# Kernel tuning notes

Hardware: AMD Instinct MI355X
Metric: run time of the kernel (lower is better)

The kernel has to match this reference:

```python
import jax, jax.numpy as jnp
import numpy as np

ALPHA = 0.5
BETA = 0.5
N_NODES = 100000
N_EDGES = 1600000
D = 64  # out_channels


def setup_inputs() -> dict:
    key = jax.random.key(0)
    ks = jax.random.split(key, 8)
    z_in = jax.random.normal(ks[0], (N_NODES, D + 1), dtype=jnp.float32)
    z_out = jax.random.normal(ks[1], (N_NODES, D + 1), dtype=jnp.float32)
    z_self = jax.random.normal(ks[2], (N_NODES, D), dtype=jnp.float32)
    edge_index = jax.random.randint(ks[3], (2, N_EDGES), 0, N_NODES, dtype=jnp.int64)
    s = 1.0 / np.sqrt(D)  # torch Linear default init scale
    W_in = jax.random.uniform(ks[4], (D, D), jnp.float32, -s, s)
    b_in = jax.random.uniform(ks[5], (D,), jnp.float32, -s, s)
    W_out = jax.random.uniform(ks[6], (D, D), jnp.float32, -s, s)
    b_out = jax.random.uniform(ks[7], (D,), jnp.float32, -s, s)
    return {"z_in": z_in, "z_out": z_out, "z_self": z_self,
            "W_in": W_in, "b_in": b_in, "W_out": W_out, "b_out": b_out,
            "edge_index": edge_index}


def _norm_degree(deg, n_unique):
    # degree / (num_unique_nodes - 1), then L2-normalize over dim 0 (F.normalize)
    d = deg / (n_unique - 1.0)
    nrm = jnp.maximum(jnp.linalg.norm(d), 1e-12)
    return d / nrm


def reference(z_in, z_out, z_self, W_in, b_in, W_out, b_out, edge_index):
    src = edge_index[0]
    dst = edge_index[1]
    n = z_self.shape[0]
    ones = jnp.ones(src.shape, jnp.float32)
    deg_out = jax.ops.segment_sum(ones, src, num_segments=n)  # out-degree per node
    deg_in = jax.ops.segment_sum(ones, dst, num_segments=n)   # in-degree per node
    present = jnp.zeros((n,), bool).at[edge_index.reshape(-1)].set(True)
    n_unique = present.sum().astype(jnp.float32)  # len(set(edge_index.flatten()))
    real_degreeout = _norm_degree(deg_out, n_unique)[src]  # [E]
    real_degreein = _norm_degree(deg_in, n_unique)[dst]    # [E]
    # small aligned linears on gathered node features
    align_out_dst = z_self[dst] @ W_out.T + b_out  # [E, D]
    align_in_src = z_self[src] @ W_in.T + b_in     # [E, D]
    value = ((real_degreeout + z_out[src, -1]) * BETA
             + jnp.sum(z_out[src, :-1] * align_out_dst, axis=1) * ALPHA
             + (real_degreein + z_in[dst, -1]) * BETA
             + jnp.sum(align_in_src * z_in[dst, :-1], axis=1) * ALPHA)
    return jax.nn.sigmoid(value)
```

## Files before the change

kernel.cpp:

```cpp
#include <hip/hip_runtime.h>
#include <hip/hip_fp16.h>
#include <math.h>

#define ALPHA_C 0.5f
#define BETA_C  0.5f
#define NPART   256
#define NQUART  4

typedef _Float16 half8 __attribute__((ext_vector_type(8)));
typedef _Float16 half2v __attribute__((ext_vector_type(2)));
typedef float f32x4 __attribute__((ext_vector_type(4)));

__device__ __forceinline__ int swz(int row, int byteoff) {
    return byteoff ^ ((row & 7) << 4);
}

__global__ __launch_bounds__(256) void k_prep(
        const float* __restrict__ W_in, const float* __restrict__ W_out,
        _Float16* __restrict__ w16i, _Float16* __restrict__ w16o) {
    for (int i = threadIdx.x; i < 4096; i += 256) {
        int k = i >> 6, n = i & 63;
        w16o[n * 64 + k] = (_Float16)W_out[k * 64 + n];
        w16i[n * 64 + k] = (_Float16)W_in [k * 64 + n];
    }
}

__global__ __launch_bounds__(256) void k_hist(
        const int* __restrict__ eidx, unsigned int* __restrict__ scr,
        int N, int E, int Q, int Wd, int chunk) {
    const int s = blockIdx.x;
    const int role = blockIdx.y;
    const int dir = role & 1;
    const int q = role >> 1;
    extern __shared__ unsigned int lds[];
    for (int w = threadIdx.x; w < Wd; w += blockDim.x) lds[w] = 0;
    __syncthreads();
    const int base = q * Q;
    const int hi = min(N - base, Q);
    const int* __restrict__ arr = eidx + (size_t)dir * E;
    const int start = s * chunk;
    const int end = min(E, start + chunk);
    const int4* __restrict__ a4 = (const int4*)arr;
    const int v1 = end >> 2;
    for (int v = (start >> 2) + threadIdx.x; v < v1; v += blockDim.x) {
        int4 x = a4[v];
        int l;
        l = x.x - base; if ((unsigned)l < (unsigned)hi) atomicAdd(&lds[l >> 1], 1u << ((l & 1) * 16));
        l = x.y - base; if ((unsigned)l < (unsigned)hi) atomicAdd(&lds[l >> 1], 1u << ((l & 1) * 16));
        l = x.z - base; if ((unsigned)l < (unsigned)hi) atomicAdd(&lds[l >> 1], 1u << ((l & 1) * 16));
        l = x.w - base; if ((unsigned)l < (unsigned)hi) atomicAdd(&lds[l >> 1], 1u << ((l & 1) * 16));
    }
    for (int i = (v1 << 2) + threadIdx.x; i < end; i += blockDim.x) {
        int l = arr[i] - base;
        if ((unsigned)l < (unsigned)hi) atomicAdd(&lds[l >> 1], 1u << ((l & 1) * 16));
    }
    __syncthreads();
    unsigned int* __restrict__ dst = scr + ((size_t)role * gridDim.x + s) * Wd;
    for (int w = threadIdx.x; w < Wd; w += blockDim.x) dst[w] = lds[w];
}

__global__ __launch_bounds__(256) void k_fold(
        const unsigned int* __restrict__ scr,
        float* __restrict__ deg_out, float* __restrict__ deg_in,
        float* __restrict__ partials, int N, int Q, int Wd, int S) {
    float so = 0.f, si = 0.f;
    for (int n = blockIdx.x * blockDim.x + threadIdx.x; n < N;
         n += gridDim.x * blockDim.x) {
        const int q = n / Q, l = n - q * Q;
        const int w = l >> 1, sh = (l & 1) * 16;
        const unsigned int* __restrict__ p0 = scr + ((size_t)(q * 2 + 0) * S) * Wd + w;
        const unsigned int* __restrict__ p1 = scr + ((size_t)(q * 2 + 1) * S) * Wd + w;
        unsigned int a = 0, b = 0;
        for (int s = 0; s < S; ++s) {
            a += (p0[(size_t)s * Wd] >> sh) & 0xFFFFu;
            b += (p1[(size_t)s * Wd] >> sh) & 0xFFFFu;
        }
        float fa = (float)a, fb = (float)b;
        deg_out[n] = fa;
        deg_in[n] = fb;
        so = fmaf(fa, fa, so);
        si = fmaf(fb, fb, si);
    }
#pragma unroll
    for (int off = 32; off; off >>= 1) {
        so += __shfl_xor(so, off);
        si += __shfl_xor(si, off);
    }
    __shared__ float sm[2][4];
    int lane = threadIdx.x & 63, w = threadIdx.x >> 6;
    if (lane == 0) { sm[0][w] = so; sm[1][w] = si; }
    __syncthreads();
    if (threadIdx.x == 0) {
        partials[blockIdx.x]         = sm[0][0] + sm[0][1] + sm[0][2] + sm[0][3];
        partials[NPART + blockIdx.x] = sm[1][0] + sm[1][1] + sm[1][2] + sm[1][3];
    }
}

__global__ __launch_bounds__(256) void k_finish(
        const float* __restrict__ partials, float* __restrict__ inv_nrm) {
    int t = threadIdx.x;
    float so = partials[t], si = partials[NPART + t];
#pragma unroll
    for (int off = 32; off; off >>= 1) {
        so += __shfl_xor(so, off);
        si += __shfl_xor(si, off);
    }
    __shared__ float sm[2][4];
    int lane = t & 63, w = t >> 6;
    if (lane == 0) { sm[0][w] = so; sm[1][w] = si; }
    __syncthreads();
    if (t == 0) {
        float a = sm[0][0] + sm[0][1] + sm[0][2] + sm[0][3];
        float b = sm[1][0] + sm[1][1] + sm[1][2] + sm[1][3];
        inv_nrm[0] = (a > 0.f) ? rsqrtf(a) : 0.f;
        inv_nrm[1] = (b > 0.f) ? rsqrtf(b) : 0.f;
    }
}

__global__ __launch_bounds__(256) void k_nodes(
        const float* __restrict__ z_in, const float* __restrict__ z_out,
        const float* __restrict__ z_self,
        const _Float16* __restrict__ w16i, const _Float16* __restrict__ w16o,
        const float* __restrict__ b_in, const float* __restrict__ b_out,
        const float* __restrict__ deg_out, const float* __restrict__ deg_in,
        const float* __restrict__ inv_nrm,
        _Float16* __restrict__ P_src, _Float16* __restrict__ P_dst,
        float* __restrict__ s_src, float* __restrict__ s_dst, int N) {
    __shared__ _Float16 smem[16384];
    char* lzo = (char*)smem;
    char* lzi = (char*)smem + 8192;
    char* lps = (char*)smem;
    char* lpd = (char*)smem + 16384;

    const int tid = threadIdx.x;
    const int lane = tid & 63;
    const int wid = tid >> 6;
    const int r = lane & 15, g = lane >> 4;
    const int base = blockIdx.x * 64;
    const int wrow = wid * 16;

#pragma unroll
    for (int it = 0; it < 8; ++it) {
        int flat = it * 256 + tid;
        int row = flat >> 5;
        int c2 = (flat & 31) * 2;
        int grow = min(base + row, N - 1);
        const float* zr = z_out + (size_t)grow * 65;
        half2v ho = { (_Float16)zr[c2], (_Float16)zr[c2 + 1] };
        *(half2v*)(lzo + row * 128 + swz(row, c2 * 2)) = ho;
        const float* zr2 = z_in + (size_t)grow * 65;
        half2v hi = { (_Float16)zr2[c2], (_Float16)zr2[c2 + 1] };
        *(half2v*)(lzi + row * 128 + swz(row, c2 * 2)) = hi;
    }
    half8 bO[2], bI[2];
#pragma unroll
    for (int s = 0; s < 2; ++s)
#pragma unroll
        for (int j = 0; j < 8; ++j) {
            int k = 32 * s + 8 * g + j;
            bO[s][j] = (r == 0) ? (_Float16)b_out[k] : (_Float16)0.f;
            bI[s][j] = (r == 0) ? (_Float16)b_in [k] : (_Float16)0.f;
        }
    __syncthreads();

    half8 AO[2], AI[2];
#pragma unroll
    for (int s = 0; s < 2; ++s) {
        int arow = wrow + r;
        int off = arow * 128 + swz(arow, s * 64 + g * 16);
        AO[s] = *(half8*)(lzo + off);
        AI[s] = *(half8*)(lzi + off);
    }
    f32x4 aO[4], aI[4], abO = (f32x4)0.f, abI = (f32x4)0.f;
#pragma unroll
    for (int t = 0; t < 4; ++t) { aO[t] = (f32x4)0.f; aI[t] = (f32x4)0.f; }
#pragma unroll
    for (int s = 0; s < 2; ++s) {
#pragma unroll
        for (int t = 0; t < 4; ++t) {
            int woff = (16 * t + r) * 64 + 32 * s + 8 * g;
            half8 BO = *(const half8*)(w16o + woff);
            aO[t] = __builtin_amdgcn_mfma_f32_16x16x32_f16(AO[s], BO, aO[t], 0, 0, 0);
            half8 BI = *(const half8*)(w16i + woff);
            aI[t] = __builtin_amdgcn_mfma_f32_16x16x32_f16(AI[s], BI, aI[t], 0, 0, 0);
        }
        abO = __builtin_amdgcn_mfma_f32_16x16x32_f16(AO[s], bO[s], abO, 0, 0, 0);
        abI = __builtin_amdgcn_mfma_f32_16x16x32_f16(AI[s], bI[s], abI, 0, 0, 0);
    }
    __syncthreads();

#pragma unroll
    for (int t = 0; t < 4; ++t)
#pragma unroll
        for (int rr = 0; rr < 4; ++rr) {
            int lrow = wrow + 4 * g + rr;
            int col2 = (16 * t + r) * 2;
            *(_Float16*)(lps + lrow * 256 + swz(lrow, col2)) = (_Float16)aO[t][rr];
            *(_Float16*)(lpd + lrow * 256 + swz(lrow, 128 + col2)) = (_Float16)aI[t][rr];
        }
#pragma unroll
    for (int it = 0; it < 8; ++it) {
        int flat = it * 256 + tid;
        int row = flat >> 5;
        int c2 = (flat & 31) * 2;
        int grow = min(base + row, N - 1);
        float2 v = *(const float2*)(z_self + (size_t)grow * 64 + c2);
        half2v h = { (_Float16)v.x, (_Float16)v.y };
        *(half2v*)(lps + row * 256 + swz(row, 128 + c2 * 2)) = h;
        *(half2v*)(lpd + row * 256 + swz(row, c2 * 2)) = h;
    }
    if (r == 0) {
        const float i0 = inv_nrm[0], i1 = inv_nrm[1];
#pragma unroll
        for (int rr = 0; rr < 4; ++rr) {
            int m = base + wrow + 4 * g + rr;
            if (m < N) {
                s_src[m] = BETA_C * fmaf(deg_out[m], i0, z_out[(size_t)m * 65 + 64])
                         + ALPHA_C * abO[rr];
                s_dst[m] = BETA_C * fmaf(deg_in[m],  i1, z_in [(size_t)m * 65 + 64])
                         + ALPHA_C * abI[rr];
            }
        }
    }
    __syncthreads();

#pragma unroll
    for (int it = 0; it < 4; ++it) {
        int lrow = it * 16 + (tid >> 4);
        int seg = tid & 15;
        int m = base + lrow;
        if (m < N) {
            half8 v = *(half8*)(lps + lrow * 256 + swz(lrow, seg * 16));
            *(half8*)(P_src + (size_t)m * 128 + seg * 8) = v;
            half8 v2 = *(half8*)(lpd + lrow * 256 + swz(lrow, seg * 16));
            *(half8*)(P_dst + (size_t)m * 128 + seg * 8) = v2;
        }
    }
}

__global__ __launch_bounds__(256) void k_edges(
        const int* __restrict__ eidx,
        const _Float16* __restrict__ P_src, const _Float16* __restrict__ P_dst,
        const float* __restrict__ s_src, const float* __restrict__ s_dst,
        float* __restrict__ out, int E) {
    const int sub = threadIdx.x & 15;
    const int grp = blockIdx.x * (blockDim.x >> 4) + (threadIdx.x >> 4);
    const int e0 = grp << 1;
    if (e0 >= E) return;
    const bool has1 = (e0 + 1) < E;
    int2 ss = *(const int2*)(eidx + e0);
    int2 dd = *(const int2*)(eidx + E + e0);
    const int s1 = has1 ? ss.y : ss.x, d1 = has1 ? dd.y : dd.x;
    const uint4 a0 = *(const uint4*)(P_src + (size_t)ss.x * 128 + sub * 8);
    const uint4 b0 = *(const uint4*)(P_dst + (size_t)dd.x * 128 + sub * 8);
    const uint4 a1 = *(const uint4*)(P_src + (size_t)s1 * 128 + sub * 8);
    const uint4 b1 = *(const uint4*)(P_dst + (size_t)d1 * 128 + sub * 8);
    float ssum = 0.f;
    if (sub < 2) {
        int s = sub ? s1 : ss.x;
        int d = sub ? d1 : dd.x;
        ssum = s_src[s] + s_dst[d];
    }
    float acc0 = 0.f, acc1 = 0.f;
    acc0 = __builtin_amdgcn_fdot2(__builtin_bit_cast(half2v, a0.x), __builtin_bit_cast(half2v, b0.x), acc0, false);
    acc0 = __builtin_amdgcn_fdot2(__builtin_bit_cast(half2v, a0.y), __builtin_bit_cast(half2v, b0.y), acc0, false);
    acc0 = __builtin_amdgcn_fdot2(__builtin_bit_cast(half2v, a0.z), __builtin_bit_cast(half2v, b0.z), acc0, false);
    acc0 = __builtin_amdgcn_fdot2(__builtin_bit_cast(half2v, a0.w), __builtin_bit_cast(half2v, b0.w), acc0, false);
    acc1 = __builtin_amdgcn_fdot2(__builtin_bit_cast(half2v, a1.x), __builtin_bit_cast(half2v, b1.x), acc1, false);
    acc1 = __builtin_amdgcn_fdot2(__builtin_bit_cast(half2v, a1.y), __builtin_bit_cast(half2v, b1.y), acc1, false);
    acc1 = __builtin_amdgcn_fdot2(__builtin_bit_cast(half2v, a1.z), __builtin_bit_cast(half2v, b1.z), acc1, false);
    acc1 = __builtin_amdgcn_fdot2(__builtin_bit_cast(half2v, a1.w), __builtin_bit_cast(half2v, b1.w), acc1, false);
#pragma unroll
    for (int off = 8; off; off >>= 1) {
        acc0 += __shfl_xor(acc0, off);
        acc1 += __shfl_xor(acc1, off);
    }
    if (sub < 2 && (sub == 0 || has1)) {
        float acc = sub ? acc1 : acc0;
        float v = fmaf(ALPHA_C, acc, ssum);
        out[e0 + sub] = 1.0f / (1.0f + __expf(-v));
    }
}

extern "C" void kernel_launch(void* const* d_in, const int* in_sizes, int n_in,
                              void* d_out, int out_size, void* d_ws, size_t ws_size,
                              hipStream_t stream) {
    const float* z_in   = (const float*)d_in[0];
    const float* z_out  = (const float*)d_in[1];
    const float* z_self = (const float*)d_in[2];
    const float* W_in   = (const float*)d_in[3];
    const float* b_in   = (const float*)d_in[4];
    const float* W_out  = (const float*)d_in[5];
    const float* b_out  = (const float*)d_in[6];
    const int*   eidx   = (const int*)d_in[7];

    const int N = in_sizes[2] / 64;
    const int E = in_sizes[7] / 2;

    const int Q = (N + NQUART - 1) / NQUART;
    const int Wd = (Q + 1) / 2;
    int S = (E + 49999) / 50000;
    if (S < 1) S = 1;
    int chunk = ((E + S - 1) / S + 3) & ~3;

    float* ws       = (float*)d_ws;
    float* deg_out  = ws;
    float* deg_in   = ws + (size_t)N;
    float* s_src    = ws + 2 * (size_t)N;
    float* s_dst    = ws + 3 * (size_t)N;
    _Float16* P_src = (_Float16*)(ws + 4 * (size_t)N);
    _Float16* P_dst = P_src + (size_t)N * 128;
    float* partials = (float*)(P_dst + (size_t)N * 128);
    float* inv_nrm  = partials + 2 * NPART;
    _Float16* w16o  = (_Float16*)(partials + 2 * NPART + 16);
    _Float16* w16i  = w16o + 4096;
    unsigned int* scr = (unsigned int*)P_src;

    k_prep<<<1, 256, 0, stream>>>(W_in, W_out, w16i, w16o);
    dim3 hgrid(S, 2 * NQUART);
    k_hist<<<hgrid, 256, (size_t)Wd * 4, stream>>>(eidx, scr, N, E, Q, Wd, chunk);
    k_fold<<<NPART, 256, 0, stream>>>(scr, deg_out, deg_in, partials, N, Q, Wd, S);
    k_finish<<<1, 256, 0, stream>>>(partials, inv_nrm);
    k_nodes<<<(N + 63) / 64, 256, 0, stream>>>(z_in, z_out, z_self, w16i, w16o,
                                               b_in, b_out, deg_out, deg_in,
                                               inv_nrm, P_src, P_dst,
                                               s_src, s_dst, N);
    {
        int groups = (E + 1) / 2;
        int blocks = (groups + 15) / 16;
        k_edges<<<blocks, 256, 0, stream>>>(eidx, P_src, P_dst,
                                            s_src, s_dst, (float*)d_out, E);
    }
}
```

Before: 212.9 us.

## Bucket edges by destination range for locality and fold weight prep into node kernel

Adds a counting pass and a scatter pass that reorder edges into eight buckets by destination-node range, packing src and the local dst offset into one word. A new edge kernel then processes each bucket so that P_dst gathers hit a smaller working set that may stay in cache. Separately, the one-block weight transpose/convert kernel is removed and each node block converts W into LDS itself. The cost is extra passes over the edge list, writes of packed indices plus permutation, and scattered output writes through eidq.

```diff
diff --git a/kernel.cpp b/kernel.cpp
--- a/kernel.cpp
+++ b/kernel.cpp
@@ -6,6 +6,8 @@
 #define BETA_C  0.5f
 #define NPART   256
 #define NQUART  4
+#define NBKT    8
+#define SCH     6250
 
 typedef _Float16 half8 __attribute__((ext_vector_type(8)));
 typedef _Float16 half2v __attribute__((ext_vector_type(2)));
@@ -13,16 +15,6 @@
 
 __device__ __forceinline__ int swz(int row, int byteoff) {
     return byteoff ^ ((row & 7) << 4);
-}
-
-__global__ __launch_bounds__(256) void k_prep(
-        const float* __restrict__ W_in, const float* __restrict__ W_out,
-        _Float16* __restrict__ w16i, _Float16* __restrict__ w16o) {
-    for (int i = threadIdx.x; i < 4096; i += 256) {
-        int k = i >> 6, n = i & 63;
-        w16o[n * 64 + k] = (_Float16)W_out[k * 64 + n];
-        w16i[n * 64 + k] = (_Float16)W_in [k * 64 + n];
-    }
 }
 
 __global__ __launch_bounds__(256) void k_hist(
@@ -57,6 +49,30 @@
     __syncthreads();
     unsigned int* __restrict__ dst = scr + ((size_t)role * gridDim.x + s) * Wd;
     for (int w = threadIdx.x; w < Wd; w += blockDim.x) dst[w] = lds[w];
+}
+
+__global__ __launch_bounds__(256) void k_bcnt(
+        const int* __restrict__ eidx, unsigned* __restrict__ wgcnt,
+        int E, int BQ) {
+    __shared__ unsigned cnt[NBKT];
+    if (threadIdx.x < NBKT) cnt[threadIdx.x] = 0;
+    __syncthreads();
+    const int c0 = blockIdx.x * SCH;
+    const int lim = min(E - c0, SCH);
+    const int lane = threadIdx.x & 63;
+    for (int it = 0; it * 256 < lim; ++it) {
+        int i = it * 256 + threadIdx.x;
+        unsigned bkt = NBKT;
+        if (i < lim) bkt = (unsigned)eidx[E + c0 + i] / (unsigned)BQ;
+#pragma unroll
+        for (unsigned b = 0; b < NBKT; ++b) {
+            unsigned long long m = __ballot(bkt == b);
+            if (m && lane == (__ffsll((long long)m) - 1))
+                atomicAdd(&cnt[b], (unsigned)__popcll(m));
+        }
+    }
+    __syncthreads();
+    if (threadIdx.x < NBKT) wgcnt[blockIdx.x * NBKT + threadIdx.x] = cnt[threadIdx.x];
 }
 
 __global__ __launch_bounds__(256) void k_fold(
@@ -97,8 +113,19 @@
 }
 
 __global__ __launch_bounds__(256) void k_finish(
-        const float* __restrict__ partials, float* __restrict__ inv_nrm) {
+        const float* __restrict__ partials, float* __restrict__ inv_nrm,
+        const unsigned* __restrict__ wgcnt, unsigned* __restrict__ wgbase,
+        unsigned* __restrict__ bmeta, int NWG) {
     int t = threadIdx.x;
+    __shared__ unsigned sb[NBKT];
+    if (t < NBKT && NWG > 0) {
+        unsigned run = 0;
+        for (int w = 0; w < NWG; ++w) {
+            wgbase[w * NBKT + t] = run;
+            run += wgcnt[w * NBKT + t];
+        }
+        sb[t] = run;
+    }
     float so = partials[t], si = partials[NPART + t];
 #pragma unroll
     for (int off = 32; off; off >>= 1) {
@@ -114,14 +141,66 @@
         float b = sm[1][0] + sm[1][1] + sm[1][2] + sm[1][3];
         inv_nrm[0] = (a > 0.f) ? rsqrtf(a) : 0.f;
         inv_nrm[1] = (b > 0.f) ? rsqrtf(b) : 0.f;
+        if (NWG > 0) {
+            unsigned acc = 0;
+#pragma unroll
+            for (int bb = 0; bb < NBKT; ++bb) {
+                bmeta[bb] = acc;
+                bmeta[NBKT + bb] = sb[bb];
+                acc += sb[bb];
+            }
+        }
+    }
+}
+
+__global__ __launch_bounds__(256) void k_scatter(
+        const int* __restrict__ eidx, const unsigned* __restrict__ wgbase,
+        const unsigned* __restrict__ bmeta, unsigned* __restrict__ packed_sd,
+        int* __restrict__ eidq, int E, int BQ) {
+    __shared__ unsigned lsd[SCH];
+    __shared__ unsigned char lb[SCH];
+    __shared__ unsigned lcur[NBKT];
+    const int w = blockIdx.x;
+    const int c0 = w * SCH;
+    const int lim = min(E - c0, SCH);
+    const int tid = threadIdx.x, lane = tid & 63;
+    if (tid < NBKT) lcur[tid] = bmeta[tid] + wgbase[w * NBKT + tid];
+    for (int it = 0; it * 256 < lim; ++it) {
+        int i = it * 256 + tid;
+        if (i < lim) {
+            unsigned s = (unsigned)eidx[c0 + i];
+            unsigned d = (unsigned)eidx[E + c0 + i];
+            unsigned b = d / (unsigned)BQ;
+            lsd[i] = s | ((d - b * (unsigned)BQ) << 17);
+            lb[i] = (unsigned char)b;
+        }
+    }
+    __syncthreads();
+    for (int it = 0; it * 256 < lim; ++it) {
+        int i = it * 256 + tid;
+        unsigned bkt = (i < lim) ? (unsigned)lb[i] : (unsigned)NBKT;
+#pragma unroll
+        for (unsigned b = 0; b < NBKT; ++b) {
+            unsigned long long m = __ballot(bkt == b);
+            if (!m) continue;
+            int leader = __ffsll((long long)m) - 1;
+            unsigned pbase = 0;
+            if (lane == leader) pbase = atomicAdd(&lcur[b], (unsigned)__popcll(m));
+            pbase = (unsigned)__shfl((int)pbase, leader);
+            if (bkt == b) {
+                unsigned pos = pbase + (unsigned)__popcll(m & ((1ULL << lane) - 1));
+                packed_sd[pos] = lsd[i];
+                eidq[pos] = c0 + i;
+            }
+        }
     }
 }
 
 __global__ __launch_bounds__(256) void k_nodes(
         const float* __restrict__ z_in, const float* __restrict__ z_out,
         const float* __restrict__ z_self,
-        const _Float16* __restrict__ w16i, const _Float16* __restrict__ w16o,
-        const float* __restrict__ b_in, const float* __restrict__ b_out,
+        const float* __restrict__ W_in, const float* __restrict__ b_in,
+        const float* __restrict__ W_out, const float* __restrict__ b_out,
         const float* __restrict__ deg_out, const float* __restrict__ deg_in,
         const float* __restrict__ inv_nrm,
         _Float16* __restrict__ P_src, _Float16* __restrict__ P_dst,
@@ -129,6 +208,8 @@
     __shared__ _Float16 smem[16384];
     char* lzo = (char*)smem;
     char* lzi = (char*)smem + 8192;
+    char* lwo = (char*)smem + 16384;
+    char* lwi = (char*)smem + 24576;
     char* lps = (char*)smem;
     char* lpd = (char*)smem + 16384;
 
@@ -152,6 +233,13 @@
         half2v hi = { (_Float16)zr2[c2], (_Float16)zr2[c2 + 1] };
         *(half2v*)(lzi + row * 128 + swz(row, c2 * 2)) = hi;
     }
+#pragma unroll
+    for (int it = 0; it < 16; ++it) {
+        int flat = it * 256 + tid;
+        int k = flat >> 6, n = flat & 63;
+        *(_Float16*)(lwo + n * 128 + swz(n, k * 2)) = (_Float16)W_out[k * 64 + n];
+        *(_Float16*)(lwi + n * 128 + swz(n, k * 2)) = (_Float16)W_in [k * 64 + n];
+    }
     half8 bO[2], bI[2];
 #pragma unroll
     for (int s = 0; s < 2; ++s)
@@ -178,10 +266,11 @@
     for (int s = 0; s < 2; ++s) {
 #pragma unroll
         for (int t = 0; t < 4; ++t) {
-            int woff = (16 * t + r) * 64 + 32 * s + 8 * g;
-            half8 BO = *(const half8*)(w16o + woff);
+            int n = 16 * t + r;
+            int off = n * 128 + swz(n, s * 64 + g * 16);
+            half8 BO = *(half8*)(lwo + off);
             aO[t] = __builtin_amdgcn_mfma_f32_16x16x32_f16(AO[s], BO, aO[t], 0, 0, 0);
-            half8 BI = *(const half8*)(w16i + woff);
+            half8 BI = *(half8*)(lwi + off);
             aI[t] = __builtin_amdgcn_mfma_f32_16x16x32_f16(AI[s], BI, aI[t], 0, 0, 0);
         }
         abO = __builtin_amdgcn_mfma_f32_16x16x32_f16(AO[s], bO[s], abO, 0, 0, 0);
@@ -234,6 +323,61 @@
             *(half8*)(P_src + (size_t)m * 128 + seg * 8) = v;
             half8 v2 = *(half8*)(lpd + lrow * 256 + swz(lrow, seg * 16));
             *(half8*)(P_dst + (size_t)m * 128 + seg * 8) = v2;
+        }
+    }
+}
+
+__global__ __launch_bounds__(256) void k_edges2(
+        const unsigned* __restrict__ packed_sd, const int* __restrict__ eidq,
+        const unsigned* __restrict__ bmeta,
+        const _Float16* __restrict__ P_src, const _Float16* __restrict__ P_dst,
+        const float* __restrict__ s_src, const float* __restrict__ s_dst,
+        float* __restrict__ out, int BQ) {
+    const int b = blockIdx.x & (NBKT - 1);
+    const unsigned base = bmeta[b], cnt = bmeta[NBKT + b];
+    const unsigned dbase = (unsigned)b * (unsigned)BQ;
+    const unsigned jstr = gridDim.x >> 3;
+    const int sub = threadIdx.x & 15;
+    const int grp = threadIdx.x >> 4;
+    for (unsigned j = blockIdx.x >> 3; j * 32 < cnt; j += jstr) {
+        unsigned i0 = j * 32 + (unsigned)grp * 2;
+        bool v0 = i0 < cnt, v1 = (i0 + 1) < cnt;
+        unsigned ce0 = base + (v0 ? i0 : 0u);
+        unsigned ce1 = base + (v1 ? i0 + 1 : (v0 ? i0 : 0u));
+        unsigned p0 = packed_sd[ce0], p1 = packed_sd[ce1];
+        int s0 = p0 & 0x1FFFF, d0 = (int)(dbase + (p0 >> 17));
+        int s1 = p1 & 0x1FFFF, d1 = (int)(dbase + (p1 >> 17));
+        const uint4 a0 = *(const uint4*)(P_src + (size_t)s0 * 128 + sub * 8);
+        const uint4 b0 = *(const uint4*)(P_dst + (size_t)d0 * 128 + sub * 8);
+        const uint4 a1 = *(const uint4*)(P_src + (size_t)s1 * 128 + sub * 8);
+        const uint4 b1 = *(const uint4*)(P_dst + (size_t)d1 * 128 + sub * 8);
+        float ssum = 0.f;
+        if (sub < 2) {
+            int s = sub ? s1 : s0;
+            int d = sub ? d1 : d0;
+            ssum = s_src[s] + s_dst[d];
+        }
+        float acc0 = 0.f, acc1 = 0.f;
+        acc0 = __builtin_amdgcn_fdot2(__builtin_bit_cast(half2v, a0.x), __builtin_bit_cast(half2v, b0.x), acc0, false);
+        acc0 = __builtin_amdgcn_fdot2(__builtin_bit_cast(half2v, a0.y), __builtin_bit_cast(half2v, b0.y), acc0, false);
+        acc0 = __builtin_amdgcn_fdot2(__builtin_bit_cast(half2v, a0.z), __builtin_bit_cast(half2v, b0.z), acc0, false);
+        acc0 = __builtin_amdgcn_fdot2(__builtin_bit_cast(half2v, a0.w), __builtin_bit_cast(half2v, b0.w), acc0, false);
+        acc1 = __builtin_amdgcn_fdot2(__builtin_bit_cast(half2v, a1.x), __builtin_bit_cast(half2v, b1.x), acc1, false);
+        acc1 = __builtin_amdgcn_fdot2(__builtin_bit_cast(half2v, a1.y), __builtin_bit_cast(half2v, b1.y), acc1, false);
+        acc1 = __builtin_amdgcn_fdot2(__builtin_bit_cast(half2v, a1.z), __builtin_bit_cast(half2v, b1.z), acc1, false);
+        acc1 = __builtin_amdgcn_fdot2(__builtin_bit_cast(half2v, a1.w), __builtin_bit_cast(half2v, b1.w), acc1, false);
+#pragma unroll
+        for (int off = 8; off; off >>= 1) {
+            acc0 += __shfl_xor(acc0, off);
+            acc1 += __shfl_xor(acc1, off);
+        }
+        if (sub == 0 && v0) {
+            float v = fmaf(ALPHA_C, acc0, ssum);
+            out[eidq[ce0]] = 1.0f / (1.0f + __expf(-v));
+        }
+        if (sub == 1 && v1) {
+            float v = fmaf(ALPHA_C, acc1, ssum);
+            out[eidq[ce1]] = 1.0f / (1.0f + __expf(-v));
         }
     }
 }
@@ -303,6 +447,9 @@
     if (S < 1) S = 1;
     int chunk = ((E + S - 1) / S + 3) & ~3;
 
+    const int BQ = (N + NBKT - 1) / NBKT;
+    const int NWG = (E + SCH - 1) / SCH;
+
     float* ws       = (float*)d_ws;
     float* deg_out  = ws;
     float* deg_in   = ws + (size_t)N;
@@ -312,20 +459,35 @@
     _Float16* P_dst = P_src + (size_t)N * 128;
     float* partials = (float*)(P_dst + (size_t)N * 128);
     float* inv_nrm  = partials + 2 * NPART;
-    _Float16* w16o  = (_Float16*)(partials + 2 * NPART + 16);
-    _Float16* w16i  = w16o + 4096;
+    unsigned* wgcnt = (unsigned*)(inv_nrm + 2);
+    unsigned* wgbase = wgcnt + (size_t)NWG * NBKT;
+    unsigned* bmeta  = wgbase + (size_t)NWG * NBKT;
+    unsigned* packed_sd = bmeta + 16;
+    int*      eidq      = (int*)(packed_sd + (size_t)E);
+    size_t need_bytes = (size_t)((char*)(eidq + (size_t)E) - (char*)d_ws);
+    const bool bucketed = (ws_size >= need_bytes) && (N <= (1 << 17));
     unsigned int* scr = (unsigned int*)P_src;
 
-    k_prep<<<1, 256, 0, stream>>>(W_in, W_out, w16i, w16o);
     dim3 hgrid(S, 2 * NQUART);
     k_hist<<<hgrid, 256, (size_t)Wd * 4, stream>>>(eidx, scr, N, E, Q, Wd, chunk);
+    if (bucketed)
+        k_bcnt<<<NWG, 256, 0, stream>>>(eidx, wgcnt, E, BQ);
     k_fold<<<NPART, 256, 0, stream>>>(scr, deg_out, deg_in, partials, N, Q, Wd, S);
-    k_finish<<<1, 256, 0, stream>>>(partials, inv_nrm);
-    k_nodes<<<(N + 63) / 64, 256, 0, stream>>>(z_in, z_out, z_self, w16i, w16o,
-                                               b_in, b_out, deg_out, deg_in,
+    k_finish<<<1, 256, 0, stream>>>(partials, inv_nrm, wgcnt, wgbase, bmeta,
+                                    bucketed ? NWG : 0);
+    if (bucketed)
+        k_scatter<<<NWG, 256, 0, stream>>>(eidx, wgbase, bmeta,
+                                           packed_sd, eidq, E, BQ);
+    k_nodes<<<(N + 63) / 64, 256, 0, stream>>>(z_in, z_out, z_self, W_in, b_in,
+                                               W_out, b_out, deg_out, deg_in,
                                                inv_nrm, P_src, P_dst,
                                                s_src, s_dst, N);
-    {
+    if (bucketed) {
+        int blocks = ((E + 31) / 32 + 7) & ~7;
+        k_edges2<<<blocks, 256, 0, stream>>>(packed_sd, eidq, bmeta,
+                                             P_src, P_dst, s_src, s_dst,
+                                             (float*)d_out, BQ);
+    } else {
         int groups = (E + 1) / 2;
         int blocks = (groups + 15) / 16;
         k_edges<<<blocks, 256, 0, stream>>>(eidx, P_src, P_dst,
```

Result: slower. 276.9 us (+30.1%).

## Fold weight prep into finish kernel, stage weights in LDS, 4 edges per group

Applied to the files above, without the earlier changes.

Removes the separate single-block weight-conversion launch by folding it into k_finish. k_nodes now stages the fp16 weight matrices in swizzled LDS instead of reading them from global memory per MFMA operand. k_edges processes four edges per 16-lane group instead of two, issuing more independent gathers per thread to raise memory-level parallelism, at the cost of more registers and scalar index loads. The LDS staging uses the upper half of the shared buffer, which later overlaps the output staging region after a sync.

```diff
diff --git a/kernel.cpp b/kernel.cpp
--- a/kernel.cpp
+++ b/kernel.cpp
@@ -13,16 +13,6 @@
 
 __device__ __forceinline__ int swz(int row, int byteoff) {
     return byteoff ^ ((row & 7) << 4);
-}
-
-__global__ __launch_bounds__(256) void k_prep(
-        const float* __restrict__ W_in, const float* __restrict__ W_out,
-        _Float16* __restrict__ w16i, _Float16* __restrict__ w16o) {
-    for (int i = threadIdx.x; i < 4096; i += 256) {
-        int k = i >> 6, n = i & 63;
-        w16o[n * 64 + k] = (_Float16)W_out[k * 64 + n];
-        w16i[n * 64 + k] = (_Float16)W_in [k * 64 + n];
-    }
 }
 
 __global__ __launch_bounds__(256) void k_hist(
@@ -97,8 +87,15 @@
 }
 
 __global__ __launch_bounds__(256) void k_finish(
-        const float* __restrict__ partials, float* __restrict__ inv_nrm) {
+        const float* __restrict__ partials, float* __restrict__ inv_nrm,
+        const float* __restrict__ W_in, const float* __restrict__ W_out,
+        _Float16* __restrict__ w16i, _Float16* __restrict__ w16o) {
     int t = threadIdx.x;
+    for (int i = t; i < 4096; i += 256) {
+        int k = i >> 6, n = i & 63;
+        w16o[n * 64 + k] = (_Float16)W_out[k * 64 + n];
+        w16i[n * 64 + k] = (_Float16)W_in [k * 64 + n];
+    }
     float so = partials[t], si = partials[NPART + t];
 #pragma unroll
     for (int off = 32; off; off >>= 1) {
@@ -129,6 +126,8 @@
     __shared__ _Float16 smem[16384];
     char* lzo = (char*)smem;
     char* lzi = (char*)smem + 8192;
+    char* lwo = (char*)smem + 16384;
+    char* lwi = (char*)smem + 24576;
     char* lps = (char*)smem;
     char* lpd = (char*)smem + 16384;
 
@@ -152,6 +151,14 @@
         half2v hi = { (_Float16)zr2[c2], (_Float16)zr2[c2 + 1] };
         *(half2v*)(lzi + row * 128 + swz(row, c2 * 2)) = hi;
     }
+#pragma unroll
+    for (int it = 0; it < 2; ++it) {
+        int flat = it * 256 + tid;
+        int n = flat >> 3;
+        int c = flat & 7;
+        *(half8*)(lwo + n * 128 + swz(n, c * 16)) = *(const half8*)(w16o + flat * 8);
+        *(half8*)(lwi + n * 128 + swz(n, c * 16)) = *(const half8*)(w16i + flat * 8);
+    }
     half8 bO[2], bI[2];
 #pragma unroll
     for (int s = 0; s < 2; ++s)
@@ -178,10 +185,11 @@
     for (int s = 0; s < 2; ++s) {
 #pragma unroll
         for (int t = 0; t < 4; ++t) {
-            int woff = (16 * t + r) * 64 + 32 * s + 8 * g;
-            half8 BO = *(const half8*)(w16o + woff);
+            int n = 16 * t + r;
+            int off = n * 128 + swz(n, s * 64 + g * 16);
+            half8 BO = *(half8*)(lwo + off);
             aO[t] = __builtin_amdgcn_mfma_f32_16x16x32_f16(AO[s], BO, aO[t], 0, 0, 0);
-            half8 BI = *(const half8*)(w16i + woff);
+            half8 BI = *(half8*)(lwi + off);
             aI[t] = __builtin_amdgcn_mfma_f32_16x16x32_f16(AI[s], BI, aI[t], 0, 0, 0);
         }
         abO = __builtin_amdgcn_mfma_f32_16x16x32_f16(AO[s], bO[s], abO, 0, 0, 0);
@@ -244,39 +252,51 @@
         const float* __restrict__ s_src, const float* __restrict__ s_dst,
         float* __restrict__ out, int E) {
     const int sub = threadIdx.x & 15;
-    const int grp = blockIdx.x * (blockDim.x >> 4) + (threadIdx.x >> 4);
-    const int e0 = grp << 1;
+    const int grp = blockIdx.x * 16 + (threadIdx.x >> 4);
+    const int e0 = grp << 2;
     if (e0 >= E) return;
-    const bool has1 = (e0 + 1) < E;
-    int2 ss = *(const int2*)(eidx + e0);
-    int2 dd = *(const int2*)(eidx + E + e0);
-    const int s1 = has1 ? ss.y : ss.x, d1 = has1 ? dd.y : dd.x;
-    const uint4 a0 = *(const uint4*)(P_src + (size_t)ss.x * 128 + sub * 8);
-    const uint4 b0 = *(const uint4*)(P_dst + (size_t)dd.x * 128 + sub * 8);
-    const uint4 a1 = *(const uint4*)(P_src + (size_t)s1 * 128 + sub * 8);
-    const uint4 b1 = *(const uint4*)(P_dst + (size_t)d1 * 128 + sub * 8);
+    int se0 = eidx[min(e0 + 0, E - 1)], de0 = eidx[E + min(e0 + 0, E - 1)];
+    int se1 = eidx[min(e0 + 1, E - 1)], de1 = eidx[E + min(e0 + 1, E - 1)];
+    int se2 = eidx[min(e0 + 2, E - 1)], de2 = eidx[E + min(e0 + 2, E - 1)];
+    int se3 = eidx[min(e0 + 3, E - 1)], de3 = eidx[E + min(e0 + 3, E - 1)];
+    const uint4 a0 = *(const uint4*)(P_src + (size_t)se0 * 128 + sub * 8);
+    const uint4 b0 = *(const uint4*)(P_dst + (size_t)de0 * 128 + sub * 8);
+    const uint4 a1 = *(const uint4*)(P_src + (size_t)se1 * 128 + sub * 8);
+    const uint4 b1 = *(const uint4*)(P_dst + (size_t)de1 * 128 + sub * 8);
+    const uint4 a2 = *(const uint4*)(P_src + (size_t)se2 * 128 + sub * 8);
+    const uint4 b2 = *(const uint4*)(P_dst + (size_t)de2 * 128 + sub * 8);
+    const uint4 a3 = *(const uint4*)(P_src + (size_t)se3 * 128 + sub * 8);
+    const uint4 b3 = *(const uint4*)(P_dst + (size_t)de3 * 128 + sub * 8);
     float ssum = 0.f;
-    if (sub < 2) {
-        int s = sub ? s1 : ss.x;
-        int d = sub ? d1 : dd.x;
+    if (sub < 4) {
+        int s = (sub == 0) ? se0 : (sub == 1) ? se1 : (sub == 2) ? se2 : se3;
+        int d = (sub == 0) ? de0 : (sub == 1) ? de1 : (sub == 2) ? de2 : de3;
         ssum = s_src[s] + s_dst[d];
     }
-    float acc0 = 0.f, acc1 = 0.f;
-    acc0 = __builtin_amdgcn_fdot2(__builtin_bit_cast(half2v, a0.x), __builtin_bit_cast(half2v, b0.x), acc0, false);
-    acc0 = __builtin_amdgcn_fdot2(__builtin_bit_cast(half2v, a0.y), __builtin_bit_cast(half2v, b0.y), acc0, false);
-    acc0 = __builtin_amdgcn_fdot2(__builtin_bit_cast(half2v, a0.z), __builtin_bit_cast(half2v, b0.z), acc0, false);
-    acc0 = __builtin_amdgcn_fdot2(__builtin_bit_cast(half2v, a0.w), __builtin_bit_cast(half2v, b0.w), acc0, false);
-    acc1 = __builtin_amdgcn_fdot2(__builtin_bit_cast(half2v, a1.x), __builtin_bit_cast(half2v, b1.x), acc1, false);
-    acc1 = __builtin_amdgcn_fdot2(__builtin_bit_cast(half2v, a1.y), __builtin_bit_cast(half2v, b1.y), acc1, false);
-    acc1 = __builtin_amdgcn_fdot2(__builtin_bit_cast(half2v, a1.z), __builtin_bit_cast(half2v, b1.z), acc1, false);
-    acc1 = __builtin_amdgcn_fdot2(__builtin_bit_cast(half2v, a1.w), __builtin_bit_cast(half2v, b1.w), acc1, false);
+#define DOT8(acc, A, B)                                                          \
+    acc = __builtin_amdgcn_fdot2(__builtin_bit_cast(half2v, A.x),                \
+                                 __builtin_bit_cast(half2v, B.x), acc, false);   \
+    acc = __builtin_amdgcn_fdot2(__builtin_bit_cast(half2v, A.y),                \
+                                 __builtin_bit_cast(half2v, B.y), acc, false);   \
+    acc = __builtin_amdgcn_fdot2(__builtin_bit_cast(half2v, A.z),                \
+                                 __builtin_bit_cast(half2v, B.z), acc, false);   \
+    acc = __builtin_amdgcn_fdot2(__builtin_bit_cast(half2v, A.w),                \
+                                 __builtin_bit_cast(half2v, B.w), acc, false)
+    float acc0 = 0.f, acc1 = 0.f, acc2 = 0.f, acc3 = 0.f;
+    DOT8(acc0, a0, b0);
+    DOT8(acc1, a1, b1);
+    DOT8(acc2, a2, b2);
+    DOT8(acc3, a3, b3);
+#undef DOT8
 #pragma unroll
     for (int off = 8; off; off >>= 1) {
         acc0 += __shfl_xor(acc0, off);
         acc1 += __shfl_xor(acc1, off);
-    }
-    if (sub < 2 && (sub == 0 || has1)) {
-        float acc = sub ? acc1 : acc0;
+        acc2 += __shfl_xor(acc2, off);
+        acc3 += __shfl_xor(acc3, off);
+    }
+    if (sub < 4 && e0 + sub < E) {
+        float acc = (sub == 0) ? acc0 : (sub == 1) ? acc1 : (sub == 2) ? acc2 : acc3;
         float v = fmaf(ALPHA_C, acc, ssum);
         out[e0 + sub] = 1.0f / (1.0f + __expf(-v));
     }
@@ -312,22 +332,20 @@
     _Float16* P_dst = P_src + (size_t)N * 128;
     float* partials = (float*)(P_dst + (size_t)N * 128);
     float* inv_nrm  = partials + 2 * NPART;
-    _Float16* w16o  = (_Float16*)(partials + 2 * NPART + 16);
+    _Float16* w16o  = (_Float16*)(inv_nrm + 2 + 12);
     _Float16* w16i  = w16o + 4096;
     unsigned int* scr = (unsigned int*)P_src;
 
-    k_prep<<<1, 256, 0, stream>>>(W_in, W_out, w16i, w16o);
     dim3 hgrid(S, 2 * NQUART);
     k_hist<<<hgrid, 256, (size_t)Wd * 4, stream>>>(eidx, scr, N, E, Q, Wd, chunk);
     k_fold<<<NPART, 256, 0, stream>>>(scr, deg_out, deg_in, partials, N, Q, Wd, S);
-    k_finish<<<1, 256, 0, stream>>>(partials, inv_nrm);
+    k_finish<<<1, 256, 0, stream>>>(partials, inv_nrm, W_in, W_out, w16i, w16o);
     k_nodes<<<(N + 63) / 64, 256, 0, stream>>>(z_in, z_out, z_self, w16i, w16o,
                                                b_in, b_out, deg_out, deg_in,
                                                inv_nrm, P_src, P_dst,
                                                s_src, s_dst, N);
     {
-        int groups = (E + 1) / 2;
-        int blocks = (groups + 15) / 16;
+        int blocks = (E + 63) / 64;
         k_edges<<<blocks, 256, 0, stream>>>(eidx, P_src, P_dst,
                                             s_src, s_dst, (float*)d_out, E);
     }
```

After: 204.3 us. 4.0% less time.

## Merge per-node src/dst projections into one shared row and stage weights in LDS

Applied to the files above, without the earlier changes.

The two per-node gather tables (P_src = [W_out·z_out, z_self], P_dst = [z_self, W_in·z_in]) become one 192-half row per node, [aO, z_self, aI], so the z_self copy is stored once. The edge kernel reads the first 128 halves of the row for the source and the last 128 for the destination. This cuts node-kernel write traffic and the memory footprint of the random edge gathers, which should improve cache hit rates. Separately, the weight transpose/convert moves from a standalone launch into k_finish, and k_nodes stages the fp16 weights in swizzled LDS instead of reading them from global memory per MFMA. The LDS weight area overlaps the output staging buffer and relies on the existing barrier between them.

```diff
diff --git a/kernel.cpp b/kernel.cpp
--- a/kernel.cpp
+++ b/kernel.cpp
@@ -13,16 +13,6 @@
 
 __device__ __forceinline__ int swz(int row, int byteoff) {
     return byteoff ^ ((row & 7) << 4);
-}
-
-__global__ __launch_bounds__(256) void k_prep(
-        const float* __restrict__ W_in, const float* __restrict__ W_out,
-        _Float16* __restrict__ w16i, _Float16* __restrict__ w16o) {
-    for (int i = threadIdx.x; i < 4096; i += 256) {
-        int k = i >> 6, n = i & 63;
-        w16o[n * 64 + k] = (_Float16)W_out[k * 64 + n];
-        w16i[n * 64 + k] = (_Float16)W_in [k * 64 + n];
-    }
 }
 
 __global__ __launch_bounds__(256) void k_hist(
@@ -97,8 +87,15 @@
 }
 
 __global__ __launch_bounds__(256) void k_finish(
-        const float* __restrict__ partials, float* __restrict__ inv_nrm) {
+        const float* __restrict__ partials, float* __restrict__ inv_nrm,
+        const float* __restrict__ W_in, const float* __restrict__ W_out,
+        _Float16* __restrict__ w16i, _Float16* __restrict__ w16o) {
     int t = threadIdx.x;
+    for (int i = t; i < 4096; i += 256) {
+        int k = i >> 6, n = i & 63;
+        w16o[n * 64 + k] = (_Float16)W_out[k * 64 + n];
+        w16i[n * 64 + k] = (_Float16)W_in [k * 64 + n];
+    }
     float so = partials[t], si = partials[NPART + t];
 #pragma unroll
     for (int off = 32; off; off >>= 1) {
@@ -124,13 +121,14 @@
         const float* __restrict__ b_in, const float* __restrict__ b_out,
         const float* __restrict__ deg_out, const float* __restrict__ deg_in,
         const float* __restrict__ inv_nrm,
-        _Float16* __restrict__ P_src, _Float16* __restrict__ P_dst,
+        _Float16* __restrict__ P,
         float* __restrict__ s_src, float* __restrict__ s_dst, int N) {
     __shared__ _Float16 smem[16384];
     char* lzo = (char*)smem;
     char* lzi = (char*)smem + 8192;
-    char* lps = (char*)smem;
-    char* lpd = (char*)smem + 16384;
+    char* lwo = (char*)smem + 16384;
+    char* lwi = (char*)smem + 24576;
+    char* lp  = (char*)smem;
 
     const int tid = threadIdx.x;
     const int lane = tid & 63;
@@ -152,6 +150,14 @@
         half2v hi = { (_Float16)zr2[c2], (_Float16)zr2[c2 + 1] };
         *(half2v*)(lzi + row * 128 + swz(row, c2 * 2)) = hi;
     }
+#pragma unroll
+    for (int it = 0; it < 2; ++it) {
+        int flat = it * 256 + tid;
+        int n = flat >> 3;
+        int c = flat & 7;
+        *(half8*)(lwo + n * 128 + swz(n, c * 16)) = *(const half8*)(w16o + flat * 8);
+        *(half8*)(lwi + n * 128 + swz(n, c * 16)) = *(const half8*)(w16i + flat * 8);
+    }
     half8 bO[2], bI[2];
 #pragma unroll
     for (int s = 0; s < 2; ++s)
@@ -178,10 +184,11 @@
     for (int s = 0; s < 2; ++s) {
 #pragma unroll
         for (int t = 0; t < 4; ++t) {
-            int woff = (16 * t + r) * 64 + 32 * s + 8 * g;
-            half8 BO = *(const half8*)(w16o + woff);
+            int n = 16 * t + r;
+            int off = n * 128 + swz(n, s * 64 + g * 16);
+            half8 BO = *(half8*)(lwo + off);
             aO[t] = __builtin_amdgcn_mfma_f32_16x16x32_f16(AO[s], BO, aO[t], 0, 0, 0);
-            half8 BI = *(const half8*)(w16i + woff);
+            half8 BI = *(half8*)(lwi + off);
             aI[t] = __builtin_amdgcn_mfma_f32_16x16x32_f16(AI[s], BI, aI[t], 0, 0, 0);
         }
         abO = __builtin_amdgcn_mfma_f32_16x16x32_f16(AO[s], bO[s], abO, 0, 0, 0);
@@ -195,8 +202,8 @@
         for (int rr = 0; rr < 4; ++rr) {
             int lrow = wrow + 4 * g + rr;
             int col2 = (16 * t + r) * 2;
-            *(_Float16*)(lps + lrow * 256 + swz(lrow, col2)) = (_Float16)aO[t][rr];
-            *(_Float16*)(lpd + lrow * 256 + swz(lrow, 128 + col2)) = (_Float16)aI[t][rr];
+            *(_Float16*)(lp + lrow * 384 + swz(lrow, col2)) = (_Float16)aO[t][rr];
+            *(_Float16*)(lp + lrow * 384 + swz(lrow, 256 + col2)) = (_Float16)aI[t][rr];
         }
 #pragma unroll
     for (int it = 0; it < 8; ++it) {
@@ -206,8 +213,7 @@
         int grow = min(base + row, N - 1);
         float2 v = *(const float2*)(z_self + (size_t)grow * 64 + c2);
         half2v h = { (_Float16)v.x, (_Float16)v.y };
-        *(half2v*)(lps + row * 256 + swz(row, 128 + c2 * 2)) = h;
-        *(half2v*)(lpd + row * 256 + swz(row, c2 * 2)) = h;
+        *(half2v*)(lp + row * 384 + swz(row, 128 + c2 * 2)) = h;
     }
     if (r == 0) {
         const float i0 = inv_nrm[0], i1 = inv_nrm[1];
@@ -225,22 +231,20 @@
     __syncthreads();
 
 #pragma unroll
-    for (int it = 0; it < 4; ++it) {
-        int lrow = it * 16 + (tid >> 4);
-        int seg = tid & 15;
+    for (int it = 0; it < 6; ++it) {
+        int flat = it * 256 + tid;
+        int lrow = flat / 24;
+        int seg = flat - lrow * 24;
         int m = base + lrow;
         if (m < N) {
-            half8 v = *(half8*)(lps + lrow * 256 + swz(lrow, seg * 16));
-            *(half8*)(P_src + (size_t)m * 128 + seg * 8) = v;
-            half8 v2 = *(half8*)(lpd + lrow * 256 + swz(lrow, seg * 16));
-            *(half8*)(P_dst + (size_t)m * 128 + seg * 8) = v2;
+            half8 v = *(half8*)(lp + lrow * 384 + swz(lrow, seg * 16));
+            *(half8*)(P + (size_t)m * 192 + seg * 8) = v;
         }
     }
 }
 
 __global__ __launch_bounds__(256) void k_edges(
-        const int* __restrict__ eidx,
-        const _Float16* __restrict__ P_src, const _Float16* __restrict__ P_dst,
+        const int* __restrict__ eidx, const _Float16* __restrict__ P,
         const float* __restrict__ s_src, const float* __restrict__ s_dst,
         float* __restrict__ out, int E) {
     const int sub = threadIdx.x & 15;
@@ -251,10 +255,10 @@
     int2 ss = *(const int2*)(eidx + e0);
     int2 dd = *(const int2*)(eidx + E + e0);
     const int s1 = has1 ? ss.y : ss.x, d1 = has1 ? dd.y : dd.x;
-    const uint4 a0 = *(const uint4*)(P_src + (size_t)ss.x * 128 + sub * 8);
-    const uint4 b0 = *(const uint4*)(P_dst + (size_t)dd.x * 128 + sub * 8);
-    const uint4 a1 = *(const uint4*)(P_src + (size_t)s1 * 128 + sub * 8);
-    const uint4 b1 = *(const uint4*)(P_dst + (size_t)d1 * 128 + sub * 8);
+    const uint4 a0 = *(const uint4*)(P + (size_t)ss.x * 192 + sub * 8);
+    const uint4 b0 = *(const uint4*)(P + (size_t)dd.x * 192 + 64 + sub * 8);
+    const uint4 a1 = *(const uint4*)(P + (size_t)s1 * 192 + sub * 8);
+    const uint4 b1 = *(const uint4*)(P + (size_t)d1 * 192 + 64 + sub * 8);
     float ssum = 0.f;
     if (sub < 2) {
         int s = sub ? s1 : ss.x;
@@ -308,27 +312,24 @@
     float* deg_in   = ws + (size_t)N;
     float* s_src    = ws + 2 * (size_t)N;
     float* s_dst    = ws + 3 * (size_t)N;
-    _Float16* P_src = (_Float16*)(ws + 4 * (size_t)N);
-    _Float16* P_dst = P_src + (size_t)N * 128;
-    float* partials = (float*)(P_dst + (size_t)N * 128);
+    _Float16* P     = (_Float16*)(ws + 4 * (size_t)N);
+    float* partials = (float*)(P + (size_t)N * 192);
     float* inv_nrm  = partials + 2 * NPART;
-    _Float16* w16o  = (_Float16*)(partials + 2 * NPART + 16);
+    _Float16* w16o  = (_Float16*)(inv_nrm + 2 + 12);
     _Float16* w16i  = w16o + 4096;
-    unsigned int* scr = (unsigned int*)P_src;
-
-    k_prep<<<1, 256, 0, stream>>>(W_in, W_out, w16i, w16o);
+    unsigned int* scr = (unsigned int*)P;
+
     dim3 hgrid(S, 2 * NQUART);
     k_hist<<<hgrid, 256, (size_t)Wd * 4, stream>>>(eidx, scr, N, E, Q, Wd, chunk);
     k_fold<<<NPART, 256, 0, stream>>>(scr, deg_out, deg_in, partials, N, Q, Wd, S);
-    k_finish<<<1, 256, 0, stream>>>(partials, inv_nrm);
+    k_finish<<<1, 256, 0, stream>>>(partials, inv_nrm, W_in, W_out, w16i, w16o);
     k_nodes<<<(N + 63) / 64, 256, 0, stream>>>(z_in, z_out, z_self, w16i, w16o,
                                                b_in, b_out, deg_out, deg_in,
-                                               inv_nrm, P_src, P_dst,
-                                               s_src, s_dst, N);
+                                               inv_nrm, P, s_src, s_dst, N);
     {
         int groups = (E + 1) / 2;
         int blocks = (groups + 15) / 16;
-        k_edges<<<blocks, 256, 0, stream>>>(eidx, P_src, P_dst,
-                                            s_src, s_dst, (float*)d_out, E);
-    }
-}
+        k_edges<<<blocks, 256, 0, stream>>>(eidx, P, s_src, s_dst,
+                                            (float*)d_out, E);
+    }
+}
```

Result: faster. 199.8 us (-6.1%).
